# Performance work log

Hardware: AMD Instinct MI355X
Metric: run time of the kernel (lower is better)

## Reference

```python
import jax, jax.numpy as jnp
import numpy as np

EMBED = 1024
HEADS = 16
HEAD_DIM = EMBED // HEADS


def setup_inputs() -> dict:
    key = jax.random.key(0)
    ks = jax.random.split(key, 8)
    N, S = 4, 2048
    inp = {
        "values": jax.random.normal(ks[0], (N, S, EMBED), dtype=jnp.float32),
        "keys": jax.random.normal(ks[1], (N, S, EMBED), dtype=jnp.float32),
        "queries": jax.random.normal(ks[2], (N, S, EMBED), dtype=jnp.float32),
        # Linear weights stored as [in, out] (torch Linear applies x @ W.T; here W already transposed)
        "W_v": jax.random.normal(ks[3], (EMBED, EMBED), dtype=jnp.float32) / np.sqrt(EMBED),
        "W_k": jax.random.normal(ks[4], (EMBED, EMBED), dtype=jnp.float32) / np.sqrt(EMBED),
        "W_q": jax.random.normal(ks[5], (EMBED, EMBED), dtype=jnp.float32) / np.sqrt(EMBED),
        "W_o": jax.random.normal(ks[6], (EMBED, EMBED), dtype=jnp.float32) / np.sqrt(EMBED),
        "b_o": jax.random.normal(ks[7], (EMBED,), dtype=jnp.float32) * 0.01,
    }
    return inp


def reference(values, keys, queries, W_v, W_k, W_q, W_o, b_o):
    N, q_len, _ = queries.shape
    v = (values @ W_v).reshape(N, -1, HEADS, HEAD_DIM)   # [n, v_len, h, d]
    k = (keys @ W_k).reshape(N, -1, HEADS, HEAD_DIM)     # [n, k_len, h, d]
    q = (queries @ W_q).reshape(N, -1, HEADS, HEAD_DIM)  # [n, q_len, h, d]
    # NOTE: original scales by sqrt(embed_size), not sqrt(head_dim)
    energy = jnp.einsum('nqhd,nkhd->nhqk', q, k) / jnp.sqrt(jnp.float32(EMBED))
    attn = jax.nn.softmax(energy, axis=-1)
    out = jnp.einsum('nhqk,nkhd->nqhd', attn, v).reshape(N, q_len, EMBED)
    return out @ W_o + b_o
```

## Files before the change

kernel.cpp:

```cpp
#include <hip/hip_runtime.h>
#include <hip/hip_bf16.h>
#include <stdint.h>

typedef __attribute__((ext_vector_type(8))) short short8;
typedef __attribute__((ext_vector_type(4))) float f32x4;
typedef __attribute__((ext_vector_type(4))) unsigned short u16x4;
typedef unsigned short u16;

#define EMBED 1024
#define SEQ 2048
#define NBATCH 4
#define MROWS (NBATCH * SEQ)

__device__ __forceinline__ u16 f2bf(float f) {
  union { float f; uint32_t u; } v; v.f = f;
  uint32_t r = v.u + 0x7fffu + ((v.u >> 16) & 1u);
  return (u16)(r >> 16);
}

__device__ __forceinline__ uint32_t cvtpk(float lo, float hi) {
  uint32_t r;
  asm("v_cvt_pk_bf16_f32 %0, %1, %2" : "=v"(r) : "v"(lo), "v"(hi));
  return r;
}

__device__ __forceinline__ float vexp2(float x) {
  float r;
  asm("v_exp_f32 %0, %1" : "=v"(r) : "v"(x));
  return r;
}

__device__ __forceinline__ void gld16(const void* g, void* l) {
  __builtin_amdgcn_global_load_lds((const __attribute__((address_space(1))) void*)g,
                                   (__attribute__((address_space(3))) void*)l, 16, 0, 0);
}

__global__ __launch_bounds__(256) void prep_kernel(const float* __restrict__ W0,
                                                   const float* __restrict__ W1,
                                                   const float* __restrict__ W2,
                                                   const float* __restrict__ W3,
                                                   u16* __restrict__ T0,
                                                   u16* __restrict__ T1,
                                                   u16* __restrict__ T2,
                                                   u16* __restrict__ T3) {
  int id = blockIdx.x;
  int z = id >> 10;
  const float* W = z == 0 ? W0 : (z == 1 ? W1 : (z == 2 ? W2 : W3));
  u16* Wt = z == 0 ? T0 : (z == 1 ? T1 : (z == 2 ? T2 : T3));
  __shared__ float tile[32][33];
  int bx = (id & 31) * 32, by = ((id >> 5) & 31) * 32;
  int tx = threadIdx.x & 31, ty = threadIdx.x >> 5;
#pragma unroll
  for (int i = 0; i < 32; i += 8)
    tile[ty + i][tx] = W[(size_t)(by + ty + i) * EMBED + bx + tx];
  __syncthreads();
#pragma unroll
  for (int i = 0; i < 32; i += 8)
    Wt[(size_t)(bx + ty + i) * EMBED + by + tx] = f2bf(tile[tx][ty + i]);
}

__global__ __launch_bounds__(256) void qkv_gemm(const float* __restrict__ Aq,
                                                const float* __restrict__ Ak,
                                                const float* __restrict__ Av,
                                                const u16* __restrict__ Wqt,
                                                const u16* __restrict__ Wkt,
                                                const u16* __restrict__ Wvt,
                                                u16* __restrict__ Qb,
                                                u16* __restrict__ Kb,
                                                u16* __restrict__ Vtb,
                                                float qscale) {
  constexpr int K = 1024;
  __shared__ float lsAf[128 * 64];
  __shared__ u16 lsB[128 * 64];

  const int id = blockIdx.x;
  const int xcd = id & 7;
  const int rest = id >> 3;
  const int bx = rest & 7;
  const int p = (rest >> 3) * 8 + xcd;
  const int z = p >> 6;
  const int by = p & 63;

  const float* A = z == 0 ? Aq : (z == 1 ? Ak : Av);
  const u16* Bt  = z == 0 ? Wqt : (z == 1 ? Wkt : Wvt);
  u16* outp      = z == 0 ? Qb : (z == 1 ? Kb : Vtb);
  const float oscale = z == 0 ? qscale : 1.0f;
  const int epi = (z == 2) ? 1 : 0;

  const int t = threadIdx.x, l = t & 63, w = t >> 6;
  const int g = l >> 4, r15 = l & 15;
  const int m0 = by * 128, n0 = bx * 128;
  const int wm = (w >> 1) * 64, wn = (w & 1) * 64;
  f32x4 acc[4][4] = {};

  const int srow = t >> 3;
  const int sc16 = (t & 7) * 16;
  const u16* Bp[4];
#pragma unroll
  for (int j = 0; j < 4; ++j) {
    int row = srow + j * 32;
    int colswz = (sc16 ^ ((row & 7) << 4)) >> 1;
    Bp[j] = Bt + (size_t)(n0 + row) * K + colswz;
  }

  const int arow_b = t >> 4;
  const int au = t & 15;
  const float* Apf[8];
#pragma unroll
  for (int j = 0; j < 8; ++j) {
    int row = j * 16 + arow_b;
    int s = ((row & 7) << 1) | ((row >> 3) & 1);
    Apf[j] = A + (size_t)(m0 + row) * K + (au ^ s) * 4;
  }

  for (int k0 = 0; k0 < K; k0 += 64) {
#pragma unroll
    for (int j = 0; j < 4; ++j)
      gld16(Bp[j] + k0, lsB + j * 2048 + w * 512);
#pragma unroll
    for (int j = 0; j < 8; ++j)
      gld16(Apf[j] + k0, (char*)lsAf + j * 4096 + w * 1024);
    __syncthreads();

    short8 af[2][4], bfv[2][4];
#pragma unroll
    for (int kk = 0; kk < 2; ++kk) {
#pragma unroll
      for (int mi = 0; mi < 4; ++mi) {
        int row = wm + mi * 16 + r15;
        int s = ((row & 7) << 1) | ((row >> 3) & 1);
        int v = kk * 8 + g * 2;
        const char* base = (const char*)lsAf + row * 256;
        f32x4 a0 = *(const f32x4*)(base + ((v ^ s) * 16));
        f32x4 a1 = *(const f32x4*)(base + (((v + 1) ^ s) * 16));
        union { uint32_t u[4]; short8 sv; } pu;
        pu.u[0] = cvtpk(a0[0], a0[1]);
        pu.u[1] = cvtpk(a0[2], a0[3]);
        pu.u[2] = cvtpk(a1[0], a1[1]);
        pu.u[3] = cvtpk(a1[2], a1[3]);
        af[kk][mi] = pu.sv;
      }
#pragma unroll
      for (int ni = 0; ni < 4; ++ni) {
        int row = wn + ni * 16 + r15;
        bfv[kk][ni] = *(const short8*)((const char*)lsB + row * 128 + ((kk * 64 + g * 16) ^ ((row & 7) << 4)));
      }
    }
#pragma unroll
    for (int kk = 0; kk < 2; ++kk)
#pragma unroll
      for (int mi = 0; mi < 4; ++mi)
#pragma unroll
        for (int ni = 0; ni < 4; ++ni)
          acc[mi][ni] = __builtin_amdgcn_mfma_f32_16x16x32_bf16(af[kk][mi], bfv[kk][ni], acc[mi][ni], 0, 0, 0);
    __syncthreads();
  }

#pragma unroll
  for (int mi = 0; mi < 4; ++mi)
#pragma unroll
    for (int ni = 0; ni < 4; ++ni)
#pragma unroll
      for (int r = 0; r < 4; ++r) {
        int row = m0 + wm + mi * 16 + g * 4 + r;
        int col = n0 + wn + ni * 16 + r15;
        float v = acc[mi][ni][r];
        if (epi == 0) {
          ((u16*)outp)[(((size_t)(row >> 11) * 16 + (col >> 6)) * SEQ + (row & 2047)) * 64 + (col & 63)] = f2bf(v * oscale);
        } else {
          ((u16*)outp)[(((size_t)(row >> 11) * 16 + (col >> 6)) * 64 + (col & 63)) * SEQ + (row & 2047)] = f2bf(v);
        }
      }
}

__global__ __launch_bounds__(256) void gemm_o(const u16* __restrict__ A,
                                              const u16* __restrict__ Bt,
                                              float* __restrict__ outp,
                                              const float* __restrict__ bias) {
  constexpr int K = 1024;
  __shared__ u16 lsA[128 * 64];
  __shared__ u16 lsB[128 * 64];

  const int id = blockIdx.x;
  const int xcd = id & 7;
  const int rest = id >> 3;
  const int bx = rest & 7;
  const int by = (rest >> 3) * 8 + xcd;

  const int t = threadIdx.x, l = t & 63, w = t >> 6;
  const int g = l >> 4, r15 = l & 15;
  const int m0 = by * 128, n0 = bx * 128;
  const int wm = (w >> 1) * 64, wn = (w & 1) * 64;
  f32x4 acc[4][4] = {};
  const int srow = t >> 3;
  const int sc16 = (t & 7) * 16;

  const u16* Ap[4]; const u16* Bp[4];
#pragma unroll
  for (int j = 0; j < 4; ++j) {
    int row = srow + j * 32;
    int colswz = (sc16 ^ ((row & 7) << 4)) >> 1;
    Ap[j] = A  + (size_t)(m0 + row) * K + colswz;
    Bp[j] = Bt + (size_t)(n0 + row) * K + colswz;
  }

  for (int k0 = 0; k0 < K; k0 += 64) {
#pragma unroll
    for (int j = 0; j < 4; ++j) {
      gld16(Ap[j] + k0, lsA + j * 2048 + w * 512);
      gld16(Bp[j] + k0, lsB + j * 2048 + w * 512);
    }
    __syncthreads();
    short8 af[2][4], bfv[2][4];
#pragma unroll
    for (int kk = 0; kk < 2; ++kk) {
#pragma unroll
      for (int mi = 0; mi < 4; ++mi) {
        int row = wm + mi * 16 + r15;
        af[kk][mi] = *(const short8*)((const char*)lsA + row * 128 + ((kk * 64 + g * 16) ^ ((row & 7) << 4)));
      }
#pragma unroll
      for (int ni = 0; ni < 4; ++ni) {
        int row = wn + ni * 16 + r15;
        bfv[kk][ni] = *(const short8*)((const char*)lsB + row * 128 + ((kk * 64 + g * 16) ^ ((row & 7) << 4)));
      }
    }
#pragma unroll
    for (int kk = 0; kk < 2; ++kk)
#pragma unroll
      for (int mi = 0; mi < 4; ++mi)
#pragma unroll
        for (int ni = 0; ni < 4; ++ni)
          acc[mi][ni] = __builtin_amdgcn_mfma_f32_16x16x32_bf16(af[kk][mi], bfv[kk][ni], acc[mi][ni], 0, 0, 0);
    __syncthreads();
  }

#pragma unroll
  for (int mi = 0; mi < 4; ++mi)
#pragma unroll
    for (int ni = 0; ni < 4; ++ni)
#pragma unroll
      for (int r = 0; r < 4; ++r) {
        int row = m0 + wm + mi * 16 + g * 4 + r;
        int col = n0 + wn + ni * 16 + r15;
        outp[(size_t)row * EMBED + col] = acc[mi][ni][r] + bias[col];
      }
}

__global__ __launch_bounds__(256) void attn_kernel(const u16* __restrict__ Q,
                                                   const u16* __restrict__ Kb,
                                                   const u16* __restrict__ Vt,
                                                   u16* __restrict__ AO) {
  __shared__ u16 lsK[3][64 * 64];
  __shared__ u16 lsV[2][64 * 64];
  const int t = threadIdx.x, l = t & 63, w = t >> 6;
  const int g = l >> 4, r15 = l & 15;

  const int flat = blockIdx.x;
  const int work = (flat & 7) * 128 + (flat >> 3);
  const int bh = work >> 4;
  const int q0 = (work & 15) * 128;

  const u16* Qh = Q + (size_t)bh * SEQ * 64;
  const u16* Kh = Kb + (size_t)bh * SEQ * 64;
  const u16* Vh = Vt + (size_t)bh * 64 * SEQ;

  short8 qf[2][2];
#pragma unroll
  for (int qi = 0; qi < 2; ++qi)
#pragma unroll
    for (int dh = 0; dh < 2; ++dh)
      qf[qi][dh] = *(const short8*)&Qh[(size_t)(q0 + w * 32 + qi * 16 + r15) * 64 + dh * 32 + g * 8];

  const short8 kones = { 0x3F80, 0x3F80, 0x3F80, 0x3F80, 0x3F80, 0x3F80, 0x3F80, 0x3F80 };
  f32x4 ssum[2] = {};
  f32x4 oacc[4][2] = {};

  const int srow = t >> 3;
  const int scolb = (t & 7) * 16;

  uint4 vreg[2][2];

  auto STAGE_K = [&](int buf, int kv0) {
#pragma unroll
    for (int j = 0; j < 2; ++j) {
      int row = j * 32 + srow;
      int colswz = (scolb ^ ((row & 7) << 4)) >> 1;
      gld16(Kh + (size_t)(kv0 + row) * 64 + colswz, &lsK[buf][j * 2048 + w * 512]);
    }
  };
  auto VLOAD = [&](int par, int kv0) {
#pragma unroll
    for (int j = 0; j < 2; ++j) {
      int row = j * 32 + srow;
      vreg[par][j] = *(const uint4*)(Vh + (size_t)row * SEQ + kv0 + (scolb >> 1));
    }
  };
  auto VSTORE = [&](int buf, int par) {
#pragma unroll
    for (int j = 0; j < 2; ++j) {
      int row = j * 32 + srow;
      int c4 = (row & 7) << 4, c3 = ((row >> 3) & 1) << 3;
      char* base = (char*)&lsV[buf][0] + row * 128 + (scolb ^ c4);
      *(uint2*)(base + c3)       = make_uint2(vreg[par][j].x, vreg[par][j].y);
      *(uint2*)(base + (8 ^ c3)) = make_uint2(vreg[par][j].z, vreg[par][j].w);
    }
  };

  auto COMPUTE = [&](const u16* Kc, const u16* Vc) {
    f32x4 sacc[2][4] = {};
    __builtin_amdgcn_s_setprio(1);
#pragma unroll
    for (int c = 0; c < 4; ++c) {
      int krow = c * 16 + r15;
      int sz = (krow & 7) << 4;
#pragma unroll
      for (int dh = 0; dh < 2; ++dh) {
        short8 kf = *(const short8*)((const char*)Kc + krow * 128 + ((dh * 64 + g * 16) ^ sz));
#pragma unroll
        for (int qi = 0; qi < 2; ++qi)
          sacc[qi][c] = __builtin_amdgcn_mfma_f32_16x16x32_bf16(kf, qf[qi][dh], sacc[qi][c], 0, 0, 0);
      }
    }
    __builtin_amdgcn_s_setprio(0);

    short8 pb[2][2];
#pragma unroll
    for (int qi = 0; qi < 2; ++qi) {
#pragma unroll
      for (int c = 0; c < 4; ++c)
#pragma unroll
        for (int r = 0; r < 4; ++r)
          sacc[qi][c][r] = vexp2(sacc[qi][c][r]);
#pragma unroll
      for (int kh = 0; kh < 2; ++kh) {
        union { uint32_t u[4]; short8 s; } pu;
        pu.u[0] = cvtpk(sacc[qi][2 * kh][0],     sacc[qi][2 * kh][1]);
        pu.u[1] = cvtpk(sacc[qi][2 * kh][2],     sacc[qi][2 * kh][3]);
        pu.u[2] = cvtpk(sacc[qi][2 * kh + 1][0], sacc[qi][2 * kh + 1][1]);
        pu.u[3] = cvtpk(sacc[qi][2 * kh + 1][2], sacc[qi][2 * kh + 1][3]);
        pb[qi][kh] = pu.s;
      }
    }
#pragma unroll
    for (int qi = 0; qi < 2; ++qi)
#pragma unroll
      for (int kh = 0; kh < 2; ++kh)
        ssum[qi] = __builtin_amdgcn_mfma_f32_16x16x32_bf16(kones, pb[qi][kh], ssum[qi], 0, 0, 0);

    __builtin_amdgcn_s_setprio(1);
#pragma unroll
    for (int dc = 0; dc < 4; ++dc) {
      int vrow = dc * 16 + r15;
      int sz = ((vrow & 7) << 4) | (((vrow >> 3) & 1) << 3);
      const char* vb = (const char*)Vc + vrow * 128;
#pragma unroll
      for (int kh = 0; kh < 2; ++kh) {
        union { uint2 v[2]; short8 s; } va;
        va.v[0] = *(const uint2*)(vb + ((kh * 64 + 8 * g) ^ sz));
        va.v[1] = *(const uint2*)(vb + ((kh * 64 + 32 + 8 * g) ^ sz));
#pragma unroll
        for (int qi = 0; qi < 2; ++qi)
          oacc[dc][qi] = __builtin_amdgcn_mfma_f32_16x16x32_bf16(va.s, pb[qi][kh], oacc[dc][qi], 0, 0, 0);
      }
    }
    __builtin_amdgcn_s_setprio(0);
  };

  auto STEP = [&](int tt, int kb, int vb, bool stv, bool ld) {
    if (stv) VSTORE((tt + 1) & 1, (tt + 1) & 1);
    if (ld) {
      VLOAD(tt & 1, (tt + 2) * 64);
      STAGE_K((tt + 2) % 3, (tt + 2) * 64);
    }
    COMPUTE(lsK[kb], lsV[vb]);
    if (tt < 31) {
      if (ld) asm volatile("s_waitcnt vmcnt(4)" ::: "memory");
      else    asm volatile("s_waitcnt vmcnt(0)" ::: "memory");
      asm volatile("s_waitcnt lgkmcnt(0)" ::: "memory");
      __builtin_amdgcn_s_barrier();
      __builtin_amdgcn_sched_barrier(0);
    }
  };

  VLOAD(0, 0);        STAGE_K(0, 0);
  VLOAD(1, 64);       STAGE_K(1, 64);
  VSTORE(0, 0);
  asm volatile("s_waitcnt vmcnt(4)" ::: "memory");
  asm volatile("s_waitcnt lgkmcnt(0)" ::: "memory");
  __builtin_amdgcn_s_barrier();
  __builtin_amdgcn_sched_barrier(0);

#pragma unroll 1
  for (int it = 0; it < 5; ++it) {
    int base = it * 6;
    STEP(base + 0, 0, 0, true, true);
    STEP(base + 1, 1, 1, true, true);
    STEP(base + 2, 2, 0, true, true);
    STEP(base + 3, 0, 1, true, true);
    STEP(base + 4, 1, 0, true, true);
    STEP(base + 5, 2, 1, true, true);
  }
  STEP(30, 0, 0, true, false);
  STEP(31, 1, 1, false, false);

  const int nb = bh >> 4, h = bh & 15;
  float inv[2] = { 1.0f / ssum[0][0], 1.0f / ssum[1][0] };
#pragma unroll
  for (int dc = 0; dc < 4; ++dc)
#pragma unroll
    for (int qi = 0; qi < 2; ++qi) {
      int q = q0 + w * 32 + qi * 16 + r15;
      int d = dc * 16 + g * 4;
      uint32_t a = cvtpk(oacc[dc][qi][0] * inv[qi], oacc[dc][qi][1] * inv[qi]);
      uint32_t b = cvtpk(oacc[dc][qi][2] * inv[qi], oacc[dc][qi][3] * inv[qi]);
      uint2* dst = (uint2*)&AO[((size_t)(nb * SEQ + q)) * EMBED + h * 64 + d];
      *dst = make_uint2(a, b);
    }
}

extern "C" void kernel_launch(void* const* d_in, const int* in_sizes, int n_in,
                              void* d_out, int out_size, void* d_ws, size_t ws_size,
                              hipStream_t stream) {
  const float* values  = (const float*)d_in[0];
  const float* keys    = (const float*)d_in[1];
  const float* queries = (const float*)d_in[2];
  const float* W_v = (const float*)d_in[3];
  const float* W_k = (const float*)d_in[4];
  const float* W_q = (const float*)d_in[5];
  const float* W_o = (const float*)d_in[6];
  const float* b_o = (const float*)d_in[7];

  const size_t XSZ = (size_t)MROWS * EMBED;
  const size_t WSZ = (size_t)EMBED * EMBED;
  u16* ws = (u16*)d_ws;
  u16* Wvt = ws;
  u16* Wkt = Wvt + WSZ;
  u16* Wqt = Wkt + WSZ;
  u16* Wot = Wqt + WSZ;
  u16* Qb  = Wot + WSZ;
  u16* Kb  = Qb + XSZ;
  u16* Vtb = Kb + XSZ;
  u16* AO  = Vtb + XSZ;

  prep_kernel<<<4096, 256, 0, stream>>>(W_v, W_k, W_q, W_o, Wvt, Wkt, Wqt, Wot);

  const float QSCALE = 0.03125f * 1.4426950408889634f;
  qkv_gemm<<<1536, 256, 0, stream>>>(queries, keys, values, Wqt, Wkt, Wvt, Qb, Kb, Vtb, QSCALE);

  attn_kernel<<<1024, 256, 0, stream>>>(Qb, Kb, Vtb, AO);

  gemm_o<<<512, 256, 0, stream>>>(AO, Wot, (float*)d_out, b_o);
}
```

Measured before the change: 209.8 us.

## Pre-convert QKV activations to bf16 in prep kernel before projection GEMM

```diff
diff --git a/kernel.cpp b/kernel.cpp
--- a/kernel.cpp
+++ b/kernel.cpp
@@ -35,7 +35,13 @@
                                    (__attribute__((address_space(3))) void*)l, 16, 0, 0);
 }
 
-__global__ __launch_bounds__(256) void prep_kernel(const float* __restrict__ W0,
+__global__ __launch_bounds__(256) void prep_kernel(const float4* __restrict__ a,
+                                                   const float4* __restrict__ b,
+                                                   const float4* __restrict__ c,
+                                                   u16x4* __restrict__ oa,
+                                                   u16x4* __restrict__ ob,
+                                                   u16x4* __restrict__ oc, int n4,
+                                                   const float* __restrict__ W0,
                                                    const float* __restrict__ W1,
                                                    const float* __restrict__ W2,
                                                    const float* __restrict__ W3,
@@ -43,25 +49,37 @@
                                                    u16* __restrict__ T1,
                                                    u16* __restrict__ T2,
                                                    u16* __restrict__ T3) {
-  int id = blockIdx.x;
-  int z = id >> 10;
-  const float* W = z == 0 ? W0 : (z == 1 ? W1 : (z == 2 ? W2 : W3));
-  u16* Wt = z == 0 ? T0 : (z == 1 ? T1 : (z == 2 ? T2 : T3));
-  __shared__ float tile[32][33];
-  int bx = (id & 31) * 32, by = ((id >> 5) & 31) * 32;
-  int tx = threadIdx.x & 31, ty = threadIdx.x >> 5;
-#pragma unroll
-  for (int i = 0; i < 32; i += 8)
-    tile[ty + i][tx] = W[(size_t)(by + ty + i) * EMBED + bx + tx];
-  __syncthreads();
-#pragma unroll
-  for (int i = 0; i < 32; i += 8)
-    Wt[(size_t)(bx + ty + i) * EMBED + by + tx] = f2bf(tile[tx][ty + i]);
-}
-
-__global__ __launch_bounds__(256) void qkv_gemm(const float* __restrict__ Aq,
-                                                const float* __restrict__ Ak,
-                                                const float* __restrict__ Av,
+  if (blockIdx.x < 1536) {
+    int which = blockIdx.x >> 9;
+    const float4* in = which == 0 ? a : (which == 1 ? b : c);
+    u16x4* out = which == 0 ? oa : (which == 1 ? ob : oc);
+    int stride = 512 * 256;
+    for (int i = (blockIdx.x & 511) * 256 + threadIdx.x; i < n4; i += stride) {
+      float4 v = in[i];
+      u16x4 o = { f2bf(v.x), f2bf(v.y), f2bf(v.z), f2bf(v.w) };
+      out[i] = o;
+    }
+  } else {
+    int id = blockIdx.x - 1536;
+    int z = id >> 10;
+    const float* W = z == 0 ? W0 : (z == 1 ? W1 : (z == 2 ? W2 : W3));
+    u16* Wt = z == 0 ? T0 : (z == 1 ? T1 : (z == 2 ? T2 : T3));
+    __shared__ float tile[32][33];
+    int bx = (id & 31) * 32, by = ((id >> 5) & 31) * 32;
+    int tx = threadIdx.x & 31, ty = threadIdx.x >> 5;
+#pragma unroll
+    for (int i = 0; i < 32; i += 8)
+      tile[ty + i][tx] = W[(size_t)(by + ty + i) * EMBED + bx + tx];
+    __syncthreads();
+#pragma unroll
+    for (int i = 0; i < 32; i += 8)
+      Wt[(size_t)(bx + ty + i) * EMBED + by + tx] = f2bf(tile[tx][ty + i]);
+  }
+}
+
+__global__ __launch_bounds__(256) void qkv_gemm(const u16* __restrict__ Xq,
+                                                const u16* __restrict__ Xk,
+                                                const u16* __restrict__ Xv,
                                                 const u16* __restrict__ Wqt,
                                                 const u16* __restrict__ Wkt,
                                                 const u16* __restrict__ Wvt,
@@ -70,7 +88,7 @@
                                                 u16* __restrict__ Vtb,
                                                 float qscale) {
   constexpr int K = 1024;
-  __shared__ float lsAf[128 * 64];
+  __shared__ u16 lsA[128 * 64];
   __shared__ u16 lsB[128 * 64];
 
   const int id = blockIdx.x;
@@ -81,9 +99,9 @@
   const int z = p >> 6;
   const int by = p & 63;
 
-  const float* A = z == 0 ? Aq : (z == 1 ? Ak : Av);
-  const u16* Bt  = z == 0 ? Wqt : (z == 1 ? Wkt : Wvt);
-  u16* outp      = z == 0 ? Qb : (z == 1 ? Kb : Vtb);
+  const u16* A  = z == 0 ? Xq : (z == 1 ? Xk : Xv);
+  const u16* Bt = z == 0 ? Wqt : (z == 1 ? Wkt : Wvt);
+  u16* outp     = z == 0 ? Qb : (z == 1 ? Kb : Vtb);
   const float oscale = z == 0 ? qscale : 1.0f;
   const int epi = (z == 2) ? 1 : 0;
 
@@ -92,53 +110,32 @@
   const int m0 = by * 128, n0 = bx * 128;
   const int wm = (w >> 1) * 64, wn = (w & 1) * 64;
   f32x4 acc[4][4] = {};
-
   const int srow = t >> 3;
   const int sc16 = (t & 7) * 16;
-  const u16* Bp[4];
+
+  const u16* Ap[4]; const u16* Bp[4];
 #pragma unroll
   for (int j = 0; j < 4; ++j) {
     int row = srow + j * 32;
     int colswz = (sc16 ^ ((row & 7) << 4)) >> 1;
+    Ap[j] = A  + (size_t)(m0 + row) * K + colswz;
     Bp[j] = Bt + (size_t)(n0 + row) * K + colswz;
   }
 
-  const int arow_b = t >> 4;
-  const int au = t & 15;
-  const float* Apf[8];
-#pragma unroll
-  for (int j = 0; j < 8; ++j) {
-    int row = j * 16 + arow_b;
-    int s = ((row & 7) << 1) | ((row >> 3) & 1);
-    Apf[j] = A + (size_t)(m0 + row) * K + (au ^ s) * 4;
-  }
-
   for (int k0 = 0; k0 < K; k0 += 64) {
 #pragma unroll
-    for (int j = 0; j < 4; ++j)
+    for (int j = 0; j < 4; ++j) {
+      gld16(Ap[j] + k0, lsA + j * 2048 + w * 512);
       gld16(Bp[j] + k0, lsB + j * 2048 + w * 512);
-#pragma unroll
-    for (int j = 0; j < 8; ++j)
-      gld16(Apf[j] + k0, (char*)lsAf + j * 4096 + w * 1024);
+    }
     __syncthreads();
-
     short8 af[2][4], bfv[2][4];
 #pragma unroll
     for (int kk = 0; kk < 2; ++kk) {
 #pragma unroll
       for (int mi = 0; mi < 4; ++mi) {
         int row = wm + mi * 16 + r15;
-        int s = ((row & 7) << 1) | ((row >> 3) & 1);
-        int v = kk * 8 + g * 2;
-        const char* base = (const char*)lsAf + row * 256;
-        f32x4 a0 = *(const f32x4*)(base + ((v ^ s) * 16));
-        f32x4 a1 = *(const f32x4*)(base + (((v + 1) ^ s) * 16));
-        union { uint32_t u[4]; short8 sv; } pu;
-        pu.u[0] = cvtpk(a0[0], a0[1]);
-        pu.u[1] = cvtpk(a0[2], a0[3]);
-        pu.u[2] = cvtpk(a1[0], a1[1]);
-        pu.u[3] = cvtpk(a1[2], a1[3]);
-        af[kk][mi] = pu.sv;
+        af[kk][mi] = *(const short8*)((const char*)lsA + row * 128 + ((kk * 64 + g * 16) ^ ((row & 7) << 4)));
       }
 #pragma unroll
       for (int ni = 0; ni < 4; ++ni) {
@@ -434,19 +431,26 @@
   const size_t XSZ = (size_t)MROWS * EMBED;
   const size_t WSZ = (size_t)EMBED * EMBED;
   u16* ws = (u16*)d_ws;
-  u16* Wvt = ws;
+  u16* Xv  = ws;
+  u16* Xk  = ws + XSZ;
+  u16* Xq  = ws + 2 * XSZ;
+  u16* Wvt = ws + 3 * XSZ;
   u16* Wkt = Wvt + WSZ;
   u16* Wqt = Wkt + WSZ;
   u16* Wot = Wqt + WSZ;
   u16* Qb  = Wot + WSZ;
   u16* Kb  = Qb + XSZ;
   u16* Vtb = Kb + XSZ;
-  u16* AO  = Vtb + XSZ;
-
-  prep_kernel<<<4096, 256, 0, stream>>>(W_v, W_k, W_q, W_o, Wvt, Wkt, Wqt, Wot);
+  u16* AO  = Xv;
+
+  int n4 = (int)(XSZ / 4);
+  prep_kernel<<<5632, 256, 0, stream>>>((const float4*)values, (const float4*)keys,
+                                        (const float4*)queries,
+                                        (u16x4*)Xv, (u16x4*)Xk, (u16x4*)Xq, n4,
+                                        W_v, W_k, W_q, W_o, Wvt, Wkt, Wqt, Wot);
 
   const float QSCALE = 0.03125f * 1.4426950408889634f;
-  qkv_gemm<<<1536, 256, 0, stream>>>(queries, keys, values, Wqt, Wkt, Wvt, Qb, Kb, Vtb, QSCALE);
+  qkv_gemm<<<1536, 256, 0, stream>>>(Xq, Xk, Xv, Wqt, Wkt, Wvt, Qb, Kb, Vtb, QSCALE);
 
   attn_kernel<<<1024, 256, 0, stream>>>(Qb, Kb, Vtb, AO);
 
```

New measurement: 218.2 us. +4.0%, slower.

## Double-buffer QKV GEMM LDS tiles with BK=32 to overlap loads and MFMA

Applied to the files above, without the earlier changes.

```diff
diff --git a/kernel.cpp b/kernel.cpp
--- a/kernel.cpp
+++ b/kernel.cpp
@@ -4,7 +4,6 @@
 
 typedef __attribute__((ext_vector_type(8))) short short8;
 typedef __attribute__((ext_vector_type(4))) float f32x4;
-typedef __attribute__((ext_vector_type(4))) unsigned short u16x4;
 typedef unsigned short u16;
 
 #define EMBED 1024
@@ -70,8 +69,8 @@
                                                 u16* __restrict__ Vtb,
                                                 float qscale) {
   constexpr int K = 1024;
-  __shared__ float lsAf[128 * 64];
-  __shared__ u16 lsB[128 * 64];
+  __shared__ float lsAf[2][128 * 32];
+  __shared__ u16   lsB[2][128 * 32];
 
   const int id = blockIdx.x;
   const int xcd = id & 7;
@@ -93,67 +92,73 @@
   const int wm = (w >> 1) * 64, wn = (w & 1) * 64;
   f32x4 acc[4][4] = {};
 
-  const int srow = t >> 3;
-  const int sc16 = (t & 7) * 16;
-  const u16* Bp[4];
+  const float* Apf[4];
 #pragma unroll
   for (int j = 0; j < 4; ++j) {
-    int row = srow + j * 32;
-    int colswz = (sc16 ^ ((row & 7) << 4)) >> 1;
-    Bp[j] = Bt + (size_t)(n0 + row) * K + colswz;
-  }
-
-  const int arow_b = t >> 4;
-  const int au = t & 15;
-  const float* Apf[8];
-#pragma unroll
-  for (int j = 0; j < 8; ++j) {
-    int row = j * 16 + arow_b;
-    int s = ((row & 7) << 1) | ((row >> 3) & 1);
-    Apf[j] = A + (size_t)(m0 + row) * K + (au ^ s) * 4;
-  }
-
-  for (int k0 = 0; k0 < K; k0 += 64) {
+    int row = j * 32 + (t >> 3);
+    Apf[j] = A + (size_t)(m0 + row) * K + (size_t)(((t & 7) ^ (row & 7)) * 4);
+  }
+  const u16* Bp[2];
+#pragma unroll
+  for (int j = 0; j < 2; ++j) {
+    int row = j * 64 + (t >> 2);
+    Bp[j] = Bt + (size_t)(n0 + row) * K + (size_t)(((t & 3) ^ (row & 3)) * 8);
+  }
+
+  auto STAGE = [&](int buf, int k0) {
 #pragma unroll
     for (int j = 0; j < 4; ++j)
-      gld16(Bp[j] + k0, lsB + j * 2048 + w * 512);
-#pragma unroll
-    for (int j = 0; j < 8; ++j)
-      gld16(Apf[j] + k0, (char*)lsAf + j * 4096 + w * 1024);
-    __syncthreads();
-
-    short8 af[2][4], bfv[2][4];
-#pragma unroll
-    for (int kk = 0; kk < 2; ++kk) {
-#pragma unroll
-      for (int mi = 0; mi < 4; ++mi) {
-        int row = wm + mi * 16 + r15;
-        int s = ((row & 7) << 1) | ((row >> 3) & 1);
-        int v = kk * 8 + g * 2;
-        const char* base = (const char*)lsAf + row * 256;
-        f32x4 a0 = *(const f32x4*)(base + ((v ^ s) * 16));
-        f32x4 a1 = *(const f32x4*)(base + (((v + 1) ^ s) * 16));
-        union { uint32_t u[4]; short8 sv; } pu;
-        pu.u[0] = cvtpk(a0[0], a0[1]);
-        pu.u[1] = cvtpk(a0[2], a0[3]);
-        pu.u[2] = cvtpk(a1[0], a1[1]);
-        pu.u[3] = cvtpk(a1[2], a1[3]);
-        af[kk][mi] = pu.sv;
-      }
-#pragma unroll
-      for (int ni = 0; ni < 4; ++ni) {
-        int row = wn + ni * 16 + r15;
-        bfv[kk][ni] = *(const short8*)((const char*)lsB + row * 128 + ((kk * 64 + g * 16) ^ ((row & 7) << 4)));
-      }
-    }
-#pragma unroll
-    for (int kk = 0; kk < 2; ++kk)
-#pragma unroll
-      for (int mi = 0; mi < 4; ++mi)
-#pragma unroll
-        for (int ni = 0; ni < 4; ++ni)
-          acc[mi][ni] = __builtin_amdgcn_mfma_f32_16x16x32_bf16(af[kk][mi], bfv[kk][ni], acc[mi][ni], 0, 0, 0);
-    __syncthreads();
+      gld16(Apf[j] + k0, (char*)&lsAf[buf][0] + j * 4096 + t * 16);
+#pragma unroll
+    for (int j = 0; j < 2; ++j)
+      gld16(Bp[j] + k0, (char*)&lsB[buf][0] + j * 4096 + t * 16);
+  };
+
+  auto COMPUTE = [&](int buf) {
+    short8 af[4], bfv[4];
+#pragma unroll
+    for (int mi = 0; mi < 4; ++mi) {
+      int row = wm + mi * 16 + r15;
+      int s = row & 7;
+      const char* base = (const char*)&lsAf[buf][0] + row * 128;
+      f32x4 a0 = *(const f32x4*)(base + (((2 * g) ^ s) * 16));
+      f32x4 a1 = *(const f32x4*)(base + (((2 * g + 1) ^ s) * 16));
+      union { uint32_t u[4]; short8 sv; } pu;
+      pu.u[0] = cvtpk(a0[0], a0[1]);
+      pu.u[1] = cvtpk(a0[2], a0[3]);
+      pu.u[2] = cvtpk(a1[0], a1[1]);
+      pu.u[3] = cvtpk(a1[2], a1[3]);
+      af[mi] = pu.sv;
+    }
+#pragma unroll
+    for (int ni = 0; ni < 4; ++ni) {
+      int row = wn + ni * 16 + r15;
+      bfv[ni] = *(const short8*)((const char*)&lsB[buf][0] + row * 64 + ((g ^ (row & 3)) * 16));
+    }
+#pragma unroll
+    for (int mi = 0; mi < 4; ++mi)
+#pragma unroll
+      for (int ni = 0; ni < 4; ++ni)
+        acc[mi][ni] = __builtin_amdgcn_mfma_f32_16x16x32_bf16(af[mi], bfv[ni], acc[mi][ni], 0, 0, 0);
+  };
+
+  STAGE(0, 0);
+  asm volatile("s_waitcnt vmcnt(0)" ::: "memory");
+  __builtin_amdgcn_s_barrier();
+
+#pragma unroll 1
+  for (int it = 0; it < 16; ++it) {
+    int k0 = it * 64;
+    STAGE(1, k0 + 32);
+    COMPUTE(0);
+    asm volatile("s_waitcnt vmcnt(0)" ::: "memory");
+    __builtin_amdgcn_s_barrier();
+    if (it < 15) STAGE(0, k0 + 64);
+    COMPUTE(1);
+    if (it < 15) {
+      asm volatile("s_waitcnt vmcnt(0)" ::: "memory");
+      __builtin_amdgcn_s_barrier();
+    }
   }
 
 #pragma unroll
```

New measurement: 213.0 us. No clear change (+1.5%).
